# Kernel optimization log

Hardware: AMD Instinct MI355X
Metric: run time of the kernel (lower is better)

Reference implementation:

```python
import jax, jax.numpy as jnp
import numpy as np

N = 256
IL_MMI = 0.02      # insertion loss MMI
IMB = 0.01         # imbalance MMI
IL_CR = 0.02       # insertion loss Crossing
CT = 0.01          # cross talk Crossing


def _mmi_matrix():
    # 2x2 MMI: sqrt(1-IL)*[[t, i r],[i r, t]] with t=sqrt((1+imb)/2), r=sqrt((1-imb)/2)
    a = np.sqrt(1.0 - IL_MMI)
    t = np.sqrt((1.0 + IMB) / 2.0)
    r = np.sqrt((1.0 - IMB) / 2.0)
    mmi2 = a * np.array([[t, 1j * r], [1j * r, t]], dtype=np.complex64)
    # block-diagonal over even pairs (0,1),(2,3),...
    return jnp.asarray(np.kron(np.eye(N // 2, dtype=np.complex64), mmi2))


def _crossing_matrix():
    # pairs start at odd index 1; rows 0 and N-1 pass through with amplitude sqrt(1-IL)*sqrt(1-CT)
    a = np.sqrt(1.0 - IL_CR)
    thru = a * np.sqrt(1.0 - CT)
    cr2 = a * np.array([[np.sqrt(CT), 1j * np.sqrt(1.0 - CT)],
                        [1j * np.sqrt(1.0 - CT), np.sqrt(CT)]], dtype=np.complex64)
    M = np.zeros((N, N), dtype=np.complex64)
    M[0, 0] = thru
    for i in range(1, N - 1, 2):
        M[i:i + 2, i:i + 2] = cr2
    if N % 2 == 0:
        M[-1, -1] = thru
    return jnp.asarray(M)


def setup_inputs() -> dict:
    key = jax.random.key(0)
    thetas = jax.random.uniform(key, (N // 2 + 2, N), dtype=jnp.float32) * (2.0 * np.pi)
    return {"thetas": thetas}


def reference(thetas):
    MMI = _mmi_matrix()
    CR = _crossing_matrix()
    phases = jnp.exp(1j * thetas)  # [N//2+2, N] complex64; diag phase-shift layers

    # arch = ht[0] @ I  (diagonal left-multiply == row scaling)
    arch0 = jnp.diag(phases[0])

    def body(arch, ph):
        # one mesh stage with trailing crossing (iterations i = 0 .. N//2-2)
        arch = MMI @ arch
        arch = ph[:, None] * arch      # ht[i+1] @ arch
        arch = MMI @ arch
        arch = CR @ arch
        return arch, None

    arch, _ = jax.lax.scan(body, arch0, phases[1:N // 2])

    # last loop iteration (i = N//2-1): no crossing
    arch = MMI @ arch
    arch = phases[N // 2][:, None] * arch
    arch = MMI @ arch
    # final phase layer ht[N//2+1]
    arch = phases[N // 2 + 1][:, None] * arch
    return arch
```

## Files before the change

kernel.cpp:

```cpp
#include <hip/hip_runtime.h>


__device__ __forceinline__ float dpp_up1(float x) {
    return __int_as_float(__builtin_amdgcn_update_dpp(
        __float_as_int(x), __float_as_int(x), 0x138, 0xf, 0xf, false));
}
__device__ __forceinline__ float dpp_dn1(float x) {
    return __int_as_float(__builtin_amdgcn_update_dpp(
        __float_as_int(x), __float_as_int(x), 0x130, 0xf, 0xf, false));
}
__device__ __forceinline__ void sincos4(float4 th, float sn[4], float cs[4]) {
    __sincosf(th.x, &sn[0], &cs[0]);
    __sincosf(th.y, &sn[1], &cs[1]);
    __sincosf(th.z, &sn[2], &cs[2]);
    __sincosf(th.w, &sn[3], &cs[3]);
}

__device__ __forceinline__ float2 cmul_pk(float2 K, float2 z) {
    float2 t;
    asm("v_pk_mul_f32 %0, %1, %2 op_sel:[0,0] op_sel_hi:[0,1]\n\t"
        "v_pk_fma_f32 %0, %1, %2, %0 op_sel:[1,1,0] op_sel_hi:[1,0,1] neg_lo:[1,0,0]"
        : "=&v"(t) : "v"(K), "v"(z));
    return t;
}
__device__ __forceinline__ float2 cfma_pk(float2 K, float2 z, float2 acc) {
    asm("v_pk_fma_f32 %0, %1, %2, %0 op_sel:[0,0,0] op_sel_hi:[0,1,1]\n\t"
        "v_pk_fma_f32 %0, %1, %2, %0 op_sel:[1,1,0] op_sel_hi:[1,0,1] neg_lo:[1,0,0]"
        : "+v"(acc) : "v"(K), "v"(z));
    return acc;
}
__device__ __forceinline__ float2 cross_pk(float2 K, float2 z, float2 p) {
    float2 t;
    asm("v_pk_mul_f32 %0, %1, %2 op_sel:[0,0] op_sel_hi:[0,1]\n\t"
        "v_pk_fma_f32 %0, %1, %3, %0 op_sel:[1,1,0] op_sel_hi:[1,0,1] neg_lo:[1,0,0]"
        : "=&v"(t) : "v"(K), "v"(z), "v"(p));
    return t;
}

__global__ __launch_bounds__(64)
void coef_kernel(const float* __restrict__ thetas,
                 float* __restrict__ coefs)
{
    const int s0   = blockIdx.x;
    const int lane = threadIdx.x;

    const float U  = 0.98f * 0.505f;
    const float W  = 0.98f * 0.495f;
    const float Gc = 0.98f * sqrtf(0.505f * 0.495f);

    float4 th = *(const float4*)(thetas + (s0 + 1) * 256 + 4 * lane);
    float s[4], c[4];
    sincos4(th, s, c);

    float4 A, B, C;
    A.x = U * c[0] - W * c[1];   A.y = U * s[0] - W * s[1];
    A.z = U * c[1] - W * c[0];   A.w = U * s[1] - W * s[0];
    B.x = -Gc * (s[0] + s[1]);   B.y = Gc * (c[0] + c[1]);
    B.z = -Gc * (s[2] + s[3]);   B.w = Gc * (c[2] + c[3]);
    C.x = U * c[2] - W * c[3];   C.y = U * s[2] - W * s[3];
    C.z = U * c[3] - W * c[2];   C.w = U * s[3] - W * s[2];

    float4* cp = (float4*)coefs;
    cp[(s0 * 3 + 0) * 64 + lane] = A;
    cp[(s0 * 3 + 1) * 64 + lane] = B;
    cp[(s0 * 3 + 2) * 64 + lane] = C;
}

__global__ __launch_bounds__(64, 1)
void group_kernel(const float* __restrict__ thetas,
                  const float* __restrict__ coefs,
                  float* __restrict__ ws)
{
    constexpr int N = 256;
    __shared__ float4 cbuf[2][1536];

    const int g    = blockIdx.x >> 8;
    const int col  = blockIdx.x & 255;
    const int lane = threadIdx.x;
    const int base = g * 8;

    const float BT = sqrtf(0.98f * 0.01f);
    const float BR = sqrtf(0.98f * 0.99f);
    const float2 CK  = make_float2(BT, BR);
    const float2 EC0 = (lane == 0)  ? make_float2(BR, 0.f) : CK;
    const float2 EC3 = (lane == 63) ? make_float2(BR, 0.f) : CK;

    float2 z0 = make_float2(0.f, 0.f), z1 = z0, z2 = z0, z3 = z0;

    {
        const int r0 = col - 4 * lane;
        if (0 <= r0 && r0 < 4) {
            float2 v = make_float2(1.f, 0.f);
            if (g == 0) {
                float s0, c0;
                __sincosf(thetas[col], &s0, &c0);
                v = make_float2(c0, s0);
            }
            if (r0 == 0) z0 = v; else if (r0 == 1) z1 = v;
            else if (r0 == 2) z2 = v; else z3 = v;
        }
    }

    auto mstep = [&](const float4& KA, const float4& KB, const float4& KC) {
        const float2 E0 = make_float2(KA.x, KA.y), F0 = make_float2(KA.z, KA.w);
        const float2 G0 = make_float2(KB.x, KB.y), G1 = make_float2(KB.z, KB.w);
        const float2 E1 = make_float2(KC.x, KC.y), F1 = make_float2(KC.z, KC.w);
        const float2 nx0 = cfma_pk(G0, z1, cmul_pk(E0, z0));
        const float2 ny0 = cfma_pk(F0, z1, cmul_pk(G0, z0));
        const float2 nx1 = cfma_pk(G1, z3, cmul_pk(E1, z2));
        const float2 ny1 = cfma_pk(F1, z3, cmul_pk(G1, z2));
        z0 = nx0; z1 = ny0; z2 = nx1; z3 = ny1;
    };
    auto crossing = [&]() {
        const float2 pv3 = make_float2(dpp_up1(z3.x), dpp_up1(z3.y));
        const float2 nv0 = make_float2(dpp_dn1(z0.x), dpp_dn1(z0.y));
        const float2 t1 = cross_pk(CK, z1, z2);
        const float2 t2 = cross_pk(CK, z2, z1);
        z0 = cross_pk(EC0, z0, pv3);
        z3 = cross_pk(EC3, z3, nv0);
        z1 = t1; z2 = t2;
    };

    auto issue_chunk = [&](int c) {
        const float4* src = (const float4*)coefs + ((base + c) * 24) * 64 + lane;
        float4* dst = &cbuf[c & 1][0];
        #pragma unroll
        for (int j = 0; j < 24; ++j)
            __builtin_amdgcn_global_load_lds(
                (const __attribute__((address_space(1))) void*)(src + j * 64),
                (__attribute__((address_space(3))) void*)(dst + j * 64),
                16, 0, 0);
    };

    issue_chunk(0);
    issue_chunk(1);
    asm volatile("s_waitcnt vmcnt(24)" ::: "memory");
    __builtin_amdgcn_sched_barrier(0);

    for (int c = 0; c < 7; ++c) {
        const int cb = c & 1;
        float4 KA[8], KB[8], KC[8];
        #pragma unroll
        for (int k = 0; k < 8; ++k) {
            const float4* p = &cbuf[cb][k * 192 + lane];
            KA[k] = p[0]; KB[k] = p[64]; KC[k] = p[128];
        }
        asm volatile("s_waitcnt lgkmcnt(0)" ::: "memory");
        __builtin_amdgcn_sched_barrier(0);
        if (c <= 5) issue_chunk(c + 2);
        #pragma unroll
        for (int k = 0; k < 8; ++k) {
            mstep(KA[k], KB[k], KC[k]);
            crossing();
        }
        if (c <= 5)
            asm volatile("s_waitcnt vmcnt(24)" ::: "memory");
        else
            asm volatile("s_waitcnt vmcnt(0)" ::: "memory");
        __builtin_amdgcn_sched_barrier(0);
    }

    {
        float4 KA[8], KB[8], KC[8];
        #pragma unroll
        for (int k = 0; k < 8; ++k) {
            const float4* p = &cbuf[1][k * 192 + lane];
            KA[k] = p[0]; KB[k] = p[64]; KC[k] = p[128];
        }
        asm volatile("s_waitcnt lgkmcnt(0)" ::: "memory");
        __builtin_amdgcn_sched_barrier(0);
        #pragma unroll
        for (int k = 0; k < 7; ++k) {
            mstep(KA[k], KB[k], KC[k]);
            crossing();
        }
        mstep(KA[7], KB[7], KC[7]);
        if (g == 0) crossing();
    }

    if (g == 1) {
        float4 thF = *(const float4*)(thetas + 129 * N + 4 * lane);
        float sn[4], cs[4];
        sincos4(thF, sn, cs);
        z0 = cmul_pk(make_float2(cs[0], sn[0]), z0);
        z1 = cmul_pk(make_float2(cs[1], sn[1]), z1);
        z2 = cmul_pk(make_float2(cs[2], sn[2]), z2);
        z3 = cmul_pk(make_float2(cs[3], sn[3]), z3);
    }

    {
        float2* pb = (float2*)(ws + (g == 0 ? 98304 : 229376));
        const int r = 4 * lane;
        pb[(r + 0) * 256 + col] = z0;
        pb[(r + 1) * 256 + col] = z1;
        pb[(r + 2) * 256 + col] = z2;
        pb[(r + 3) * 256 + col] = z3;
    }
}

__global__ __launch_bounds__(256)
void combine_kernel(const float* __restrict__ ws,
                    float* __restrict__ out)
{
    const int c  = threadIdx.x;
    const int r0 = blockIdx.x * 2;

    const float2* A = (const float2*)(ws + 229376);
    const float2* B = (const float2*)(ws + 98304);
    const float2* a0p = A + (size_t)r0 * 256;
    const float2* a1p = A + (size_t)(r0 + 1) * 256;
    const float2* bp  = B + c;

    float ar0 = 0.f, ai0 = 0.f, ar1 = 0.f, ai1 = 0.f;
    #pragma unroll 8
    for (int k = 0; k < 256; ++k) {
        const float2 a0 = a0p[k];
        const float2 a1 = a1p[k];
        const float2 b  = bp[(size_t)k * 256];
        ar0 += a0.x * b.x - a0.y * b.y;
        ai0 += a0.x * b.y + a0.y * b.x;
        ar1 += a1.x * b.x - a1.y * b.y;
        ai1 += a1.x * b.y + a1.y * b.x;
    }

    const int i0 = r0 * 256 + c;
    out[i0]               = ar0;
    out[65536 + i0]       = ai0;
    out[i0 + 256]         = ar1;
    out[65536 + i0 + 256] = ai1;
}

extern "C" void kernel_launch(void* const* d_in, const int* in_sizes, int n_in,
                              void* d_out, int out_size, void* d_ws, size_t ws_size,
                              hipStream_t stream)
{
    const float* thetas = (const float*)d_in[0];
    float* out = (float*)d_out;
    float* ws  = (float*)d_ws;
    (void)in_sizes; (void)n_in; (void)out_size; (void)ws_size;

    coef_kernel   <<<dim3(128), dim3(64),  0, stream>>>(thetas, ws);
    group_kernel  <<<dim3(512), dim3(64),  0, stream>>>(thetas, ws, ws);
    combine_kernel<<<dim3(128), dim3(256), 0, stream>>>(ws, out);
}
```

Measured before the change: 81.92 us.

## Fuse coef, group and combine kernels into one cooperative kernel with grid syncs

Merges the three launches into a single cooperative kernel of 512 single-wave blocks that uses grid.sync between the coefficient, mesh-propagation and matrix-combine phases. This removes two kernel launch boundaries and their gaps. The combine phase is remapped to 512 blocks of 64 threads, each doing one row and two column slices using packed complex FMA. The trade-offs are grid-wide barrier cost, a cooperative launch that requires every block to be co-resident, and a smaller per-block combine that re-reads the A row in each block.

```diff
diff --git a/kernel.cpp b/kernel.cpp
--- a/kernel.cpp
+++ b/kernel.cpp
@@ -1,4 +1,7 @@
 #include <hip/hip_runtime.h>
+#include <hip/hip_cooperative_groups.h>
+
+namespace cg = cooperative_groups;
 
 
 __device__ __forceinline__ float dpp_up1(float x) {
@@ -37,197 +40,184 @@
     return t;
 }
 
-__global__ __launch_bounds__(64)
-void coef_kernel(const float* __restrict__ thetas,
-                 float* __restrict__ coefs)
+__global__ __launch_bounds__(64, 1)
+void fused_kernel(const float* __restrict__ thetas,
+                  float* __restrict__ ws,
+                  float* __restrict__ out)
 {
-    const int s0   = blockIdx.x;
+    constexpr int N = 256;
+    __shared__ float4 cbuf[2][1536];
+
+    cg::grid_group grid = cg::this_grid();
+
+    const int j    = blockIdx.x;
     const int lane = threadIdx.x;
 
     const float U  = 0.98f * 0.505f;
     const float W  = 0.98f * 0.495f;
     const float Gc = 0.98f * sqrtf(0.505f * 0.495f);
-
-    float4 th = *(const float4*)(thetas + (s0 + 1) * 256 + 4 * lane);
-    float s[4], c[4];
-    sincos4(th, s, c);
-
-    float4 A, B, C;
-    A.x = U * c[0] - W * c[1];   A.y = U * s[0] - W * s[1];
-    A.z = U * c[1] - W * c[0];   A.w = U * s[1] - W * s[0];
-    B.x = -Gc * (s[0] + s[1]);   B.y = Gc * (c[0] + c[1]);
-    B.z = -Gc * (s[2] + s[3]);   B.w = Gc * (c[2] + c[3]);
-    C.x = U * c[2] - W * c[3];   C.y = U * s[2] - W * s[3];
-    C.z = U * c[3] - W * c[2];   C.w = U * s[3] - W * s[2];
-
-    float4* cp = (float4*)coefs;
-    cp[(s0 * 3 + 0) * 64 + lane] = A;
-    cp[(s0 * 3 + 1) * 64 + lane] = B;
-    cp[(s0 * 3 + 2) * 64 + lane] = C;
-}
-
-__global__ __launch_bounds__(64, 1)
-void group_kernel(const float* __restrict__ thetas,
-                  const float* __restrict__ coefs,
-                  float* __restrict__ ws)
-{
-    constexpr int N = 256;
-    __shared__ float4 cbuf[2][1536];
-
-    const int g    = blockIdx.x >> 8;
-    const int col  = blockIdx.x & 255;
-    const int lane = threadIdx.x;
-    const int base = g * 8;
-
     const float BT = sqrtf(0.98f * 0.01f);
     const float BR = sqrtf(0.98f * 0.99f);
-    const float2 CK  = make_float2(BT, BR);
-    const float2 EC0 = (lane == 0)  ? make_float2(BR, 0.f) : CK;
-    const float2 EC3 = (lane == 63) ? make_float2(BR, 0.f) : CK;
-
-    float2 z0 = make_float2(0.f, 0.f), z1 = z0, z2 = z0, z3 = z0;
+
+    if (j < 128) {
+        float4 th = *(const float4*)(thetas + (j + 1) * 256 + 4 * lane);
+        float s[4], c[4];
+        sincos4(th, s, c);
+        float4 A, B, C;
+        A.x = U * c[0] - W * c[1];   A.y = U * s[0] - W * s[1];
+        A.z = U * c[1] - W * c[0];   A.w = U * s[1] - W * s[0];
+        B.x = -Gc * (s[0] + s[1]);   B.y = Gc * (c[0] + c[1]);
+        B.z = -Gc * (s[2] + s[3]);   B.w = Gc * (c[2] + c[3]);
+        C.x = U * c[2] - W * c[3];   C.y = U * s[2] - W * s[3];
+        C.z = U * c[3] - W * c[2];   C.w = U * s[3] - W * s[2];
+        float4* cp = (float4*)ws;
+        cp[(j * 3 + 0) * 64 + lane] = A;
+        cp[(j * 3 + 1) * 64 + lane] = B;
+        cp[(j * 3 + 2) * 64 + lane] = C;
+    }
+    grid.sync();
 
     {
-        const int r0 = col - 4 * lane;
-        if (0 <= r0 && r0 < 4) {
-            float2 v = make_float2(1.f, 0.f);
-            if (g == 0) {
-                float s0, c0;
-                __sincosf(thetas[col], &s0, &c0);
-                v = make_float2(c0, s0);
-            }
-            if (r0 == 0) z0 = v; else if (r0 == 1) z1 = v;
-            else if (r0 == 2) z2 = v; else z3 = v;
+        const int g    = j >> 8;
+        const int col  = j & 255;
+        const int base = g * 8;
+        const float* coefs = ws;
+
+        const float2 CK  = make_float2(BT, BR);
+        const float2 EC0 = (lane == 0)  ? make_float2(BR, 0.f) : CK;
+        const float2 EC3 = (lane == 63) ? make_float2(BR, 0.f) : CK;
+
+        float2 z0 = make_float2(0.f, 0.f), z1 = z0, z2 = z0, z3 = z0;
+        {
+            const int r0 = col - 4 * lane;
+            if (0 <= r0 && r0 < 4) {
+                float2 v = make_float2(1.f, 0.f);
+                if (g == 0) {
+                    float s0, c0;
+                    __sincosf(thetas[col], &s0, &c0);
+                    v = make_float2(c0, s0);
+                }
+                if (r0 == 0) z0 = v; else if (r0 == 1) z1 = v;
+                else if (r0 == 2) z2 = v; else z3 = v;
+            }
+        }
+
+        auto mstep = [&](const float4& KA, const float4& KB, const float4& KC) {
+            const float2 E0 = make_float2(KA.x, KA.y), F0 = make_float2(KA.z, KA.w);
+            const float2 G0 = make_float2(KB.x, KB.y), G1 = make_float2(KB.z, KB.w);
+            const float2 E1 = make_float2(KC.x, KC.y), F1 = make_float2(KC.z, KC.w);
+            const float2 nx0 = cfma_pk(G0, z1, cmul_pk(E0, z0));
+            const float2 ny0 = cfma_pk(F0, z1, cmul_pk(G0, z0));
+            const float2 nx1 = cfma_pk(G1, z3, cmul_pk(E1, z2));
+            const float2 ny1 = cfma_pk(F1, z3, cmul_pk(G1, z2));
+            z0 = nx0; z1 = ny0; z2 = nx1; z3 = ny1;
+        };
+        auto crossing = [&]() {
+            const float2 pv3 = make_float2(dpp_up1(z3.x), dpp_up1(z3.y));
+            const float2 nv0 = make_float2(dpp_dn1(z0.x), dpp_dn1(z0.y));
+            const float2 t1 = cross_pk(CK, z1, z2);
+            const float2 t2 = cross_pk(CK, z2, z1);
+            z0 = cross_pk(EC0, z0, pv3);
+            z3 = cross_pk(EC3, z3, nv0);
+            z1 = t1; z2 = t2;
+        };
+        auto issue_chunk = [&](int c) {
+            const float4* src = (const float4*)coefs + ((base + c) * 24) * 64 + lane;
+            float4* dst = &cbuf[c & 1][0];
+            #pragma unroll
+            for (int q = 0; q < 24; ++q)
+                __builtin_amdgcn_global_load_lds(
+                    (const __attribute__((address_space(1))) void*)(src + q * 64),
+                    (__attribute__((address_space(3))) void*)(dst + q * 64),
+                    16, 0, 0);
+        };
+
+        issue_chunk(0);
+        issue_chunk(1);
+        asm volatile("s_waitcnt vmcnt(24)" ::: "memory");
+        __builtin_amdgcn_sched_barrier(0);
+
+        for (int c = 0; c < 7; ++c) {
+            const int cb = c & 1;
+            float4 KA[8], KB[8], KC[8];
+            #pragma unroll
+            for (int k = 0; k < 8; ++k) {
+                const float4* p = &cbuf[cb][k * 192 + lane];
+                KA[k] = p[0]; KB[k] = p[64]; KC[k] = p[128];
+            }
+            asm volatile("s_waitcnt lgkmcnt(0)" ::: "memory");
+            __builtin_amdgcn_sched_barrier(0);
+            if (c <= 5) issue_chunk(c + 2);
+            #pragma unroll
+            for (int k = 0; k < 8; ++k) {
+                mstep(KA[k], KB[k], KC[k]);
+                crossing();
+            }
+            if (c <= 5)
+                asm volatile("s_waitcnt vmcnt(24)" ::: "memory");
+            else
+                asm volatile("s_waitcnt vmcnt(0)" ::: "memory");
+            __builtin_amdgcn_sched_barrier(0);
+        }
+        {
+            float4 KA[8], KB[8], KC[8];
+            #pragma unroll
+            for (int k = 0; k < 8; ++k) {
+                const float4* p = &cbuf[1][k * 192 + lane];
+                KA[k] = p[0]; KB[k] = p[64]; KC[k] = p[128];
+            }
+            asm volatile("s_waitcnt lgkmcnt(0)" ::: "memory");
+            __builtin_amdgcn_sched_barrier(0);
+            #pragma unroll
+            for (int k = 0; k < 7; ++k) {
+                mstep(KA[k], KB[k], KC[k]);
+                crossing();
+            }
+            mstep(KA[7], KB[7], KC[7]);
+            if (g == 0) crossing();
+        }
+        if (g == 1) {
+            float4 thF = *(const float4*)(thetas + 129 * N + 4 * lane);
+            float sn[4], cs[4];
+            sincos4(thF, sn, cs);
+            z0 = cmul_pk(make_float2(cs[0], sn[0]), z0);
+            z1 = cmul_pk(make_float2(cs[1], sn[1]), z1);
+            z2 = cmul_pk(make_float2(cs[2], sn[2]), z2);
+            z3 = cmul_pk(make_float2(cs[3], sn[3]), z3);
+        }
+        {
+            float2* pb = (float2*)(ws + (g == 0 ? 98304 : 229376));
+            const int r = 4 * lane;
+            pb[(r + 0) * 256 + col] = z0;
+            pb[(r + 1) * 256 + col] = z1;
+            pb[(r + 2) * 256 + col] = z2;
+            pb[(r + 3) * 256 + col] = z3;
         }
     }
-
-    auto mstep = [&](const float4& KA, const float4& KB, const float4& KC) {
-        const float2 E0 = make_float2(KA.x, KA.y), F0 = make_float2(KA.z, KA.w);
-        const float2 G0 = make_float2(KB.x, KB.y), G1 = make_float2(KB.z, KB.w);
-        const float2 E1 = make_float2(KC.x, KC.y), F1 = make_float2(KC.z, KC.w);
-        const float2 nx0 = cfma_pk(G0, z1, cmul_pk(E0, z0));
-        const float2 ny0 = cfma_pk(F0, z1, cmul_pk(G0, z0));
-        const float2 nx1 = cfma_pk(G1, z3, cmul_pk(E1, z2));
-        const float2 ny1 = cfma_pk(F1, z3, cmul_pk(G1, z2));
-        z0 = nx0; z1 = ny0; z2 = nx1; z3 = ny1;
-    };
-    auto crossing = [&]() {
-        const float2 pv3 = make_float2(dpp_up1(z3.x), dpp_up1(z3.y));
-        const float2 nv0 = make_float2(dpp_dn1(z0.x), dpp_dn1(z0.y));
-        const float2 t1 = cross_pk(CK, z1, z2);
-        const float2 t2 = cross_pk(CK, z2, z1);
-        z0 = cross_pk(EC0, z0, pv3);
-        z3 = cross_pk(EC3, z3, nv0);
-        z1 = t1; z2 = t2;
-    };
-
-    auto issue_chunk = [&](int c) {
-        const float4* src = (const float4*)coefs + ((base + c) * 24) * 64 + lane;
-        float4* dst = &cbuf[c & 1][0];
-        #pragma unroll
-        for (int j = 0; j < 24; ++j)
-            __builtin_amdgcn_global_load_lds(
-                (const __attribute__((address_space(1))) void*)(src + j * 64),
-                (__attribute__((address_space(3))) void*)(dst + j * 64),
-                16, 0, 0);
-    };
-
-    issue_chunk(0);
-    issue_chunk(1);
-    asm volatile("s_waitcnt vmcnt(24)" ::: "memory");
-    __builtin_amdgcn_sched_barrier(0);
-
-    for (int c = 0; c < 7; ++c) {
-        const int cb = c & 1;
-        float4 KA[8], KB[8], KC[8];
-        #pragma unroll
-        for (int k = 0; k < 8; ++k) {
-            const float4* p = &cbuf[cb][k * 192 + lane];
-            KA[k] = p[0]; KB[k] = p[64]; KC[k] = p[128];
-        }
-        asm volatile("s_waitcnt lgkmcnt(0)" ::: "memory");
-        __builtin_amdgcn_sched_barrier(0);
-        if (c <= 5) issue_chunk(c + 2);
-        #pragma unroll
-        for (int k = 0; k < 8; ++k) {
-            mstep(KA[k], KB[k], KC[k]);
-            crossing();
-        }
-        if (c <= 5)
-            asm volatile("s_waitcnt vmcnt(24)" ::: "memory");
-        else
-            asm volatile("s_waitcnt vmcnt(0)" ::: "memory");
-        __builtin_amdgcn_sched_barrier(0);
+    grid.sync();
+
+    {
+        const int r  = j >> 1;
+        const int c0 = (j & 1) * 128 + lane;
+        const float2* A = (const float2*)(ws + 229376) + (size_t)r * 256;
+        const float2* B = (const float2*)(ws + 98304);
+
+        float2 acc0 = make_float2(0.f, 0.f);
+        float2 acc1 = make_float2(0.f, 0.f);
+        #pragma unroll 8
+        for (int k = 0; k < 256; ++k) {
+            const float2 a  = A[k];
+            const float2 b0 = B[(size_t)k * 256 + c0];
+            const float2 b1 = B[(size_t)k * 256 + c0 + 64];
+            acc0 = cfma_pk(a, b0, acc0);
+            acc1 = cfma_pk(a, b1, acc1);
+        }
+        const int i0 = r * 256 + c0;
+        out[i0]              = acc0.x;
+        out[65536 + i0]      = acc0.y;
+        out[i0 + 64]         = acc1.x;
+        out[65536 + i0 + 64] = acc1.y;
     }
-
-    {
-        float4 KA[8], KB[8], KC[8];
-        #pragma unroll
-        for (int k = 0; k < 8; ++k) {
-            const float4* p = &cbuf[1][k * 192 + lane];
-            KA[k] = p[0]; KB[k] = p[64]; KC[k] = p[128];
-        }
-        asm volatile("s_waitcnt lgkmcnt(0)" ::: "memory");
-        __builtin_amdgcn_sched_barrier(0);
-        #pragma unroll
-        for (int k = 0; k < 7; ++k) {
-            mstep(KA[k], KB[k], KC[k]);
-            crossing();
-        }
-        mstep(KA[7], KB[7], KC[7]);
-        if (g == 0) crossing();
-    }
-
-    if (g == 1) {
-        float4 thF = *(const float4*)(thetas + 129 * N + 4 * lane);
-        float sn[4], cs[4];
-        sincos4(thF, sn, cs);
-        z0 = cmul_pk(make_float2(cs[0], sn[0]), z0);
-        z1 = cmul_pk(make_float2(cs[1], sn[1]), z1);
-        z2 = cmul_pk(make_float2(cs[2], sn[2]), z2);
-        z3 = cmul_pk(make_float2(cs[3], sn[3]), z3);
-    }
-
-    {
-        float2* pb = (float2*)(ws + (g == 0 ? 98304 : 229376));
-        const int r = 4 * lane;
-        pb[(r + 0) * 256 + col] = z0;
-        pb[(r + 1) * 256 + col] = z1;
-        pb[(r + 2) * 256 + col] = z2;
-        pb[(r + 3) * 256 + col] = z3;
-    }
-}
-
-__global__ __launch_bounds__(256)
-void combine_kernel(const float* __restrict__ ws,
-                    float* __restrict__ out)
-{
-    const int c  = threadIdx.x;
-    const int r0 = blockIdx.x * 2;
-
-    const float2* A = (const float2*)(ws + 229376);
-    const float2* B = (const float2*)(ws + 98304);
-    const float2* a0p = A + (size_t)r0 * 256;
-    const float2* a1p = A + (size_t)(r0 + 1) * 256;
-    const float2* bp  = B + c;
-
-    float ar0 = 0.f, ai0 = 0.f, ar1 = 0.f, ai1 = 0.f;
-    #pragma unroll 8
-    for (int k = 0; k < 256; ++k) {
-        const float2 a0 = a0p[k];
-        const float2 a1 = a1p[k];
-        const float2 b  = bp[(size_t)k * 256];
-        ar0 += a0.x * b.x - a0.y * b.y;
-        ai0 += a0.x * b.y + a0.y * b.x;
-        ar1 += a1.x * b.x - a1.y * b.y;
-        ai1 += a1.x * b.y + a1.y * b.x;
-    }
-
-    const int i0 = r0 * 256 + c;
-    out[i0]               = ar0;
-    out[65536 + i0]       = ai0;
-    out[i0 + 256]         = ar1;
-    out[65536 + i0 + 256] = ai1;
 }
 
 extern "C" void kernel_launch(void* const* d_in, const int* in_sizes, int n_in,
@@ -239,7 +229,7 @@
     float* ws  = (float*)d_ws;
     (void)in_sizes; (void)n_in; (void)out_size; (void)ws_size;
 
-    coef_kernel   <<<dim3(128), dim3(64),  0, stream>>>(thetas, ws);
-    group_kernel  <<<dim3(512), dim3(64),  0, stream>>>(thetas, ws, ws);
-    combine_kernel<<<dim3(128), dim3(256), 0, stream>>>(ws, out);
-}
+    void* args[] = { (void*)&thetas, (void*)&ws, (void*)&out };
+    hipLaunchCooperativeKernel((void*)fused_kernel, dim3(512), dim3(64),
+                               args, 0, stream);
+}
```

After: 207.5 us. 2.53x slower.
